# Kernel tuning notes

Hardware: AMD Instinct MI355X
Metric: run time of the kernel (lower is better)

The kernel has to match this reference:

```python
import jax, jax.numpy as jnp
import numpy as np

V = 49152      # HEALPix nside=64 pixel count
B = 2
FIN = 32
FOUT = 64
K = 8          # Chebyshev kernel_size
DEG = 8        # neighbors per pixel (plus self-loop -> 9 nnz/row)
G = 8          # GroupNorm num_groups
EPS = 1e-5
SLOPE = 0.1    # LeakyReLU negative slope


def setup_inputs() -> dict:
    key = jax.random.key(0)
    ks = jax.random.split(key, 4)
    rng = np.random.default_rng(0)
    # sparse Laplacian in COO: 8 random neighbors + self-loop per node
    row = np.repeat(np.arange(V, dtype=np.int32), DEG + 1)
    nbrs = rng.integers(0, V, size=(V, DEG))
    col = np.concatenate([nbrs, np.arange(V)[:, None]], axis=1).astype(np.int32).reshape(-1)
    vals = (rng.standard_normal(V * (DEG + 1)).astype(np.float32)) * 0.1
    x = jax.random.normal(ks[0], (B, V, FIN), dtype=jnp.float32)
    W1 = jax.random.normal(ks[1], (K, FIN, FOUT), dtype=jnp.float32) * 0.05
    W2 = jax.random.normal(ks[2], (K, FOUT, FOUT), dtype=jnp.float32) * 0.05
    Wr = jax.random.normal(ks[3], (K, FIN, FOUT), dtype=jnp.float32) * 0.05
    zeros = jnp.zeros((FOUT,), dtype=jnp.float32)
    ones = jnp.ones((FOUT,), dtype=jnp.float32)
    return {
        "x": x,
        "lap_vals": jnp.asarray(vals),
        "lap_row": jnp.asarray(row),
        "lap_col": jnp.asarray(col),
        "W1": W1, "b1": zeros, "g1": ones, "be1": zeros,
        "W2": W2, "b2": zeros, "g2": ones, "be2": zeros,
        "Wr": Wr, "br": zeros,
    }


def _spmm(vals, row, col, z):
    # L @ z for COO Laplacian; z: [V, D]
    return jax.ops.segment_sum(vals[:, None] * z[col], row, num_segments=V)


def _cheb_conv(x, vals, row, col, W, b):
    # x: [B, V, Fin], W: [K, Fin, Fout] -> [B, V, Fout]
    Bb, Vv, F = x.shape
    x0 = jnp.transpose(x, (1, 0, 2)).reshape(Vv, Bb * F)  # [V, B*F]
    xs = [x0, _spmm(vals, row, col, x0)]
    for _ in range(K - 2):
        xs.append(2.0 * _spmm(vals, row, col, xs[-1]) - xs[-2])
    Xk = jnp.stack(xs, 0).reshape(K, Vv, Bb, F)
    Xk = jnp.transpose(Xk, (2, 1, 0, 3))  # [B, V, K, F]
    return jnp.einsum('bvkf,kfo->bvo', Xk, W) + b


def _group_norm(x, gamma, beta):
    # equivalent to nn.GroupNorm applied on x.permute(0,2,1): normalize over (C/G, V)
    Bb, Vv, C = x.shape
    xg = x.reshape(Bb, Vv, G, C // G)
    mu = xg.mean(axis=(1, 3), keepdims=True)
    var = xg.var(axis=(1, 3), keepdims=True)
    xn = ((xg - mu) * jax.lax.rsqrt(var + EPS)).reshape(Bb, Vv, C)
    return xn * gamma + beta


def _block(x, vals, row, col, W, b, gamma, beta):
    h = _cheb_conv(x, vals, row, col, W, b)
    h = _group_norm(h, gamma, beta)
    return jax.nn.leaky_relu(h, SLOPE)  # out_channels > 1 -> LeakyReLU(0.1)


def reference(x, lap_vals, lap_row, lap_col, W1, b1, g1, be1, W2, b2, g2, be2, Wr, br):
    h = _block(x, lap_vals, lap_row, lap_col, W1, b1, g1, be1)
    h = _block(h, lap_vals, lap_row, lap_col, W2, b2, g2, be2)
    res = _cheb_conv(x, lap_vals, lap_row, lap_col, Wr, br)  # in != out -> res_conv
    return h + res
```

## Files before the change

kernel.cpp:

```cpp
#include <hip/hip_runtime.h>
#include <hip/hip_bf16.h>

#define V 49152
#define NNZ 9
#define EPSV 1e-5f
#define SLOPE 0.1f
#define RST 68

typedef __attribute__((ext_vector_type(8))) short bf16x8;
typedef __attribute__((ext_vector_type(4))) float f32x4;

__device__ __forceinline__ float lo2f(unsigned u) { return __uint_as_float(u << 16); }
__device__ __forceinline__ float hi2f(unsigned u) { return __uint_as_float(u & 0xffff0000u); }
__device__ __forceinline__ unsigned short f2us(float f) {
    __hip_bfloat16 h = __float2bfloat16(f);
    return *(unsigned short*)&h;
}
__device__ __forceinline__ unsigned pk2(float a, float b) {
    return ((unsigned)f2us(a)) | (((unsigned)f2us(b)) << 16);
}
__device__ __forceinline__ void fma8(float* t, float a, uint4 u) {
    t[0] += a * lo2f(u.x); t[1] += a * hi2f(u.x);
    t[2] += a * lo2f(u.y); t[3] += a * hi2f(u.y);
    t[4] += a * lo2f(u.z); t[5] += a * hi2f(u.z);
    t[6] += a * lo2f(u.w); t[7] += a * hi2f(u.w);
}
__device__ __forceinline__ void fold8(float* t, uint4 p) {
    t[0] = 2.f*t[0] - lo2f(p.x); t[1] = 2.f*t[1] - hi2f(p.x);
    t[2] = 2.f*t[2] - lo2f(p.y); t[3] = 2.f*t[3] - hi2f(p.y);
    t[4] = 2.f*t[4] - lo2f(p.z); t[5] = 2.f*t[5] - hi2f(p.z);
    t[6] = 2.f*t[6] - lo2f(p.w); t[7] = 2.f*t[7] - hi2f(p.w);
}
__device__ __forceinline__ uint4 pack8(const float* t) {
    uint4 r;
    r.x = pk2(t[0], t[1]); r.y = pk2(t[2], t[3]);
    r.z = pk2(t[4], t[5]); r.w = pk2(t[6], t[7]);
    return r;
}
__device__ __forceinline__ void gnleaky8(uint4 u, const float* scl, const float* sft, float* y) {
    float e[8] = { lo2f(u.x), hi2f(u.x), lo2f(u.y), hi2f(u.y),
                   lo2f(u.z), hi2f(u.z), lo2f(u.w), hi2f(u.w) };
    #pragma unroll
    for (int i = 0; i < 8; ++i) {
        float t = e[i] * scl[i] + sft[i];
        y[i] = t > 0.f ? t : SLOPE * t;
    }
}
__device__ __forceinline__ void gload_lds16(const void* g, void* l) {
    __builtin_amdgcn_global_load_lds((__attribute__((address_space(1))) void*)g,
                                     (__attribute__((address_space(3))) void*)l, 16, 0, 0);
}

__global__ __launch_bounds__(256) void prep_reorder_k(
    const float* __restrict__ x, unsigned* __restrict__ t0,
    const float* __restrict__ W1, const float* __restrict__ Wr, const float* __restrict__ W2,
    unsigned short* __restrict__ Wt1, unsigned short* __restrict__ Wtr, unsigned short* __restrict__ Wt2,
    float* __restrict__ part)
{
    int bid = blockIdx.x;
    if (bid < 6144) {
        int idx = bid * 256 + threadIdx.x;
        int v = idx >> 5, j2 = idx & 31;
        int b = j2 >> 4, f0 = (j2 & 15) * 2;
        const float* p = x + ((size_t)b * V + v) * 32 + f0;
        t0[idx] = pk2(p[0], p[1]);
    } else {
        int i = (bid - 6144) * 256 + threadIdx.x;
        if (i < 32768) {
            int kk = i >> 12, rem = i & 4095, o = rem >> 6, f = rem & 63;
            Wt2[i] = f2us(W2[kk * 4096 + f * 64 + o]);
        } else if (i < 49152) {
            int j = i - 32768;
            int kk = j >> 11, rem = j & 2047, o = rem >> 5, f = rem & 31;
            Wt1[j] = f2us(W1[kk * 2048 + f * 64 + o]);
        } else if (i < 65536) {
            int j = i - 49152;
            int kk = j >> 11, rem = j & 2047, o = rem >> 5, f = rem & 31;
            Wtr[j] = f2us(Wr[kk * 2048 + f * 64 + o]);
        } else if (i < 66560) {
            part[i - 65536] = 0.f;
        }
    }
}

template<int THR, bool FIRST>
__global__ __launch_bounds__(256) void spmm_step(
    const uint4* __restrict__ zc, const uint4* __restrict__ zp, uint4* __restrict__ zn,
    const float* __restrict__ vals, const int* __restrict__ col)
{
    constexpr int L4 = THR * 2;
    int tid = blockIdx.x * 256 + threadIdx.x;
    int v = tid / THR;
    int c = (tid - v * THR) * 2;
    int base = v * NNZ;
    float t[16];
    #pragma unroll
    for (int i = 0; i < 16; ++i) t[i] = 0.f;
    #pragma unroll
    for (int n = 0; n < NNZ; ++n) {
        float a = vals[base + n];
        int cc = col[base + n];
        const uint4* p = zc + (size_t)cc * L4 + c;
        fma8(t, a, p[0]);
        fma8(t + 8, a, p[1]);
    }
    if (!FIRST) {
        const uint4* pp = zp + (size_t)v * L4 + c;
        fold8(t, pp[0]);
        fold8(t + 8, pp[1]);
    }
    uint4* q = zn + (size_t)v * L4 + c;
    q[0] = pack8(t);
    q[1] = pack8(t + 8);
}

template<int MODE>
__global__ __launch_bounds__(256) void spmm2_gn(
    const unsigned short* __restrict__ ACC, const uint4* __restrict__ zc,
    uint4* __restrict__ zn, const float* __restrict__ part,
    const float* __restrict__ gamma, const float* __restrict__ beta,
    const float* __restrict__ vals, const int* __restrict__ col)
{
    int tid = blockIdx.x * 256 + threadIdx.x;
    int v = tid >> 3;
    int c2 = (tid & 7) * 2;
    int b = c2 >> 3;
    int ch0 = (c2 & 7) * 8;
    const float Nf = (float)V * 8.f;
    int g0 = c2 & 7;
    float m0 = part[(b*8+g0)*2] / Nf;
    float r0 = rsqrtf(part[(b*8+g0)*2+1]/Nf - m0*m0 + EPSV);
    float m1 = part[(b*8+g0+1)*2] / Nf;
    float r1 = rsqrtf(part[(b*8+g0+1)*2+1]/Nf - m1*m1 + EPSV);
    float scl[16], sft[16];
    #pragma unroll
    for (int i = 0; i < 8; ++i) {
        int o = ch0 + i;
        scl[i] = r0 * gamma[o];     sft[i] = beta[o] - m0 * scl[i];
        scl[8+i] = r1 * gamma[o+8]; sft[8+i] = beta[o+8] - m1 * scl[8+i];
    }

    float t[16];
    #pragma unroll
    for (int i = 0; i < 16; ++i) t[i] = 0.f;
    int base = v * NNZ;
    #pragma unroll
    for (int n = 0; n < NNZ; ++n) {
        float a = vals[base + n];
        int cc = col[base + n];
        if constexpr (MODE == 0) {
            const uint4* p = (const uint4*)(const void*)(ACC + ((size_t)b * V + cc) * 64 + ch0);
            float y[8];
            gnleaky8(p[0], scl, sft, y);
            #pragma unroll
            for (int i = 0; i < 8; ++i) t[i] += a * y[i];
            gnleaky8(p[1], scl + 8, sft + 8, y);
            #pragma unroll
            for (int i = 0; i < 8; ++i) t[8 + i] += a * y[i];
        } else {
            const uint4* p = zc + (size_t)cc * 16 + c2;
            fma8(t, a, p[0]);
            fma8(t + 8, a, p[1]);
        }
    }
    if constexpr (MODE == 1) {
        const uint4* pp = (const uint4*)(const void*)(ACC + ((size_t)b * V + v) * 64 + ch0);
        float y[8];
        gnleaky8(pp[0], scl, sft, y);
        #pragma unroll
        for (int i = 0; i < 8; ++i) t[i] = 2.f * t[i] - y[i];
        gnleaky8(pp[1], scl + 8, sft + 8, y);
        #pragma unroll
        for (int i = 0; i < 8; ++i) t[8 + i] = 2.f * t[8 + i] - y[i];
    }
    uint4* q = zn + (size_t)v * 16 + c2;
    q[0] = pack8(t);
    q[1] = pack8(t + 8);
}

__global__ __launch_bounds__(256) void gemm1f(
    const unsigned short* __restrict__ T,
    const unsigned short* __restrict__ WtA, const unsigned short* __restrict__ WtB,
    const float* __restrict__ biasA, const float* __restrict__ biasB,
    const float* __restrict__ vals, const int* __restrict__ col,
    unsigned short* __restrict__ ACC, float* __restrict__ resOut, float* __restrict__ part)
{
    __shared__ unsigned short shraw[34816];
    __shared__ float sGrp[32];
    unsigned short* tile = shraw;
    float* accbuf  = (float*)shraw;
    float* dualbuf = accbuf + 2 * 64 * RST;

    int wv = threadIdx.x >> 6, lane = threadIdx.x & 63;
    int quad = lane >> 4, l15 = lane & 15;
    int v0 = blockIdx.x * 64;
    int ot = wv;

    #pragma unroll
    for (int i = 0; i < 14; ++i) {
        int s = (i * 4 + wv) * 64 + lane;
        int kkl = s >> 9;
        int ws = s & 511;
        int row = ws >> 3;
        int cl = ws & 7;
        int cg = cl ^ (row & 7);
        const unsigned short* gp = T + ((size_t)kkl * V + v0 + row) * 64 + cg * 8;
        gload_lds16(gp, tile + (size_t)(i * 4 + wv) * 64 * 8);
    }

    {
        const unsigned short* T6 = T + (size_t)6 * V * 64;
        const unsigned short* T5 = T + (size_t)5 * V * 64;
        int row = threadIdx.x >> 2, c2 = (threadIdx.x & 3) * 2;
        int gv = v0 + row;
        float t[16];
        #pragma unroll
        for (int i = 0; i < 16; ++i) t[i] = 0.f;
        int base = gv * NNZ;
        #pragma unroll
        for (int n = 0; n < NNZ; ++n) {
            float a = vals[base + n];
            int cc = col[base + n];
            const uint4* p = (const uint4*)(const void*)(T6 + (size_t)cc * 64 + c2 * 8);
            fma8(t, a, p[0]);
            fma8(t + 8, a, p[1]);
        }
        const uint4* pp = (const uint4*)(const void*)(T5 + (size_t)gv * 64 + c2 * 8);
        fold8(t, pp[0]);
        fold8(t + 8, pp[1]);
        uint4* tl = (uint4*)tile;
        int r7 = row & 7;
        tl[(7 * 64 + row) * 8 + (c2 ^ r7)]       = pack8(t);
        tl[(7 * 64 + row) * 8 + ((c2 + 1) ^ r7)] = pack8(t + 8);
    }

    bf16x8 bw[8], bd[8];
    #pragma unroll
    for (int kk = 0; kk < 8; ++kk) {
        size_t brow = ((size_t)kk * 64 + ot * 16 + l15) * 32 + quad * 8;
        bw[kk] = *(const bf16x8*)(const void*)(WtA + brow);
        bd[kk] = *(const bf16x8*)(const void*)(WtB + brow);
    }
    f32x4 acc[4][2], accd[4][2];
    #pragma unroll
    for (int m = 0; m < 4; ++m)
        #pragma unroll
        for (int b = 0; b < 2; ++b) {
            acc[m][b]  = (f32x4){0.f, 0.f, 0.f, 0.f};
            accd[m][b] = (f32x4){0.f, 0.f, 0.f, 0.f};
        }
    __syncthreads();

    #pragma unroll
    for (int kk = 0; kk < 8; ++kk) {
        #pragma unroll
        for (int m = 0; m < 4; ++m) {
            int r = m * 16 + l15;
            int rx = r & 7;
            const unsigned short* rbase = tile + ((size_t)kk * 64 + r) * 64;
            #pragma unroll
            for (int b = 0; b < 2; ++b) {
                int s0 = (b * 4 + quad) ^ rx;
                bf16x8 a = *(const bf16x8*)(const void*)(rbase + s0 * 8);
                acc[m][b]  = __builtin_amdgcn_mfma_f32_16x16x32_bf16(a, bw[kk], acc[m][b], 0, 0, 0);
                accd[m][b] = __builtin_amdgcn_mfma_f32_16x16x32_bf16(a, bd[kk], accd[m][b], 0, 0, 0);
            }
        }
    }

    __syncthreads();
    int o = ot * 16 + l15;
    float biA = biasA[o], biB = biasB[o];
    #pragma unroll
    for (int m = 0; m < 4; ++m)
        #pragma unroll
        for (int b = 0; b < 2; ++b)
            #pragma unroll
            for (int rr = 0; rr < 4; ++rr) {
                int r = m * 16 + quad * 4 + rr;
                accbuf[(b * 64 + r) * RST + o] = acc[m][b][rr] + biA;
                dualbuf[(b * 64 + r) * RST + o] = accd[m][b][rr] + biB;
            }
    if (threadIdx.x < 32) sGrp[threadIdx.x] = 0.f;
    __syncthreads();
    #pragma unroll
    for (int j = 0; j < 4; ++j) {
        int cid = threadIdx.x + 256 * j;
        int g = cid & 7, r = (cid >> 3) & 63, b = cid >> 9;
        const float* src = accbuf + (b * 64 + r) * RST + g * 8;
        float e[8], s = 0.f, q = 0.f;
        #pragma unroll
        for (int i = 0; i < 8; ++i) { e[i] = src[i]; s += e[i]; q += e[i] * e[i]; }
        *(uint4*)(void*)(ACC + ((size_t)b * V + v0 + r) * 64 + g * 8) = pack8(e);
        atomicAdd(&sGrp[b * 8 + g], s);
        atomicAdd(&sGrp[16 + b * 8 + g], q);
    }
    #pragma unroll
    for (int j = 0; j < 8; ++j) {
        int cid = threadIdx.x + 256 * j;
        int oc = cid & 15, r = (cid >> 4) & 63, b = cid >> 10;
        float4 vv = *(const float4*)(const void*)(dualbuf + (b * 64 + r) * RST + oc * 4);
        *(float4*)(void*)(resOut + ((size_t)b * V + v0 + r) * 64 + oc * 4) = vv;
    }
    __syncthreads();
    if (threadIdx.x < 16) {
        atomicAdd(&part[threadIdx.x * 2],     sGrp[threadIdx.x]);
        atomicAdd(&part[threadIdx.x * 2 + 1], sGrp[16 + threadIdx.x]);
    }
}

__global__ __launch_bounds__(256) void gemm2f(
    const unsigned short* __restrict__ T,
    unsigned short* ACC,
    const float* __restrict__ part1, const float* __restrict__ g1, const float* __restrict__ be1,
    const unsigned short* __restrict__ Wt2, const float* __restrict__ biasA,
    float* __restrict__ part2,
    const float* __restrict__ vals, const int* __restrict__ col)
{
    __shared__ unsigned short shraw[32768];
    __shared__ float sGrp[32];
    unsigned short* tile = shraw;
    float* accbuf = (float*)shraw;

    int wv = threadIdx.x >> 6, lane = threadIdx.x & 63;
    int quad = lane >> 4, l15 = lane & 15;
    int v0 = blockIdx.x * 64;
    int ot = wv;
    const float Nf = (float)V * 8.f;

    #pragma unroll
    for (int i = 4; i < 16; ++i) {
        int s = (i * 4 + wv) * 64 + lane;
        int kkl = s >> 10;
        int ws = s & 1023;
        int row = ws >> 4;
        int cl = ws & 15;
        int cg = (cl & ~7) | ((cl & 7) ^ (row & 7));
        const unsigned short* gp = T + ((size_t)kkl * V + v0 + row) * 128 + cg * 8;
        gload_lds16(gp, tile + (size_t)(i * 4 + wv) * 64 * 8);
    }
    {
        int cl = threadIdx.x & 15;
        int b = cl >> 3, g = cl & 7, j8 = b * 8 + g;
        float mean = part1[j8 * 2] / Nf;
        float rstd = rsqrtf(part1[j8 * 2 + 1] / Nf - mean * mean + EPSV);
        int o0 = g * 8;
        float scl[8], sft[8];
        #pragma unroll
        for (int i = 0; i < 8; ++i) {
            scl[i] = rstd * g1[o0 + i];
            sft[i] = be1[o0 + i] - mean * scl[i];
        }
        uint4* tl = (uint4*)tile;
        #pragma unroll
        for (int j = 0; j < 4; ++j) {
            int r = (threadIdx.x >> 4) + 16 * j;
            uint4 aa = *(const uint4*)(const void*)(ACC + ((size_t)b * V + v0 + r) * 64 + o0);
            float y[8];
            gnleaky8(aa, scl, sft, y);
            tl[r * 16 + ((cl & ~7) | ((cl & 7) ^ (r & 7)))] = pack8(y);
        }
    }
    bf16x8 bw[8][2];
    #pragma unroll
    for (int kk = 0; kk < 8; ++kk)
        #pragma unroll
        for (int fh = 0; fh < 2; ++fh) {
            size_t brow = ((size_t)kk * 64 + ot * 16 + l15) * 64 + fh * 32 + quad * 8;
            bw[kk][fh] = *(const bf16x8*)(const void*)(Wt2 + brow);
        }
    f32x4 acc[4][2];
    #pragma unroll
    for (int m = 0; m < 4; ++m)
        #pragma unroll
        for (int b = 0; b < 2; ++b) acc[m][b] = (f32x4){0.f, 0.f, 0.f, 0.f};
    __syncthreads();

    #pragma unroll
    for (int kkl = 0; kkl < 4; ++kkl) {
        #pragma unroll
        for (int m = 0; m < 4; ++m) {
            int r = m * 16 + l15, rx = r & 7;
            const unsigned short* rbase = tile + ((size_t)kkl * 64 + r) * 128;
            #pragma unroll
            for (int b = 0; b < 2; ++b)
                #pragma unroll
                for (int fh = 0; fh < 2; ++fh) {
                    int c0 = b * 8 + fh * 4 + quad;
                    int s0 = (c0 & ~7) | ((c0 & 7) ^ rx);
                    bf16x8 a = *(const bf16x8*)(const void*)(rbase + s0 * 8);
                    acc[m][b] = __builtin_amdgcn_mfma_f32_16x16x32_bf16(a, bw[kkl][fh], acc[m][b], 0, 0, 0);
                }
        }
    }
    __syncthreads();

    #pragma unroll
    for (int i = 0; i < 12; ++i) {
        int s = (i * 4 + wv) * 64 + lane;
        int kkl = s >> 10;
        int ws = s & 1023;
        int row = ws >> 4;
        int cl = ws & 15;
        int cg = (cl & ~7) | ((cl & 7) ^ (row & 7));
        const unsigned short* gp = T + ((size_t)(4 + kkl) * V + v0 + row) * 128 + cg * 8;
        gload_lds16(gp, tile + (size_t)(i * 4 + wv) * 64 * 8);
    }
    {
        const unsigned short* T6 = T + (size_t)6 * V * 128;
        const unsigned short* T5 = T + (size_t)5 * V * 128;
        int row = threadIdx.x >> 2, cb = (threadIdx.x & 3) * 4;
        int gv = v0 + row;
        float t[32];
        #pragma unroll
        for (int i = 0; i < 32; ++i) t[i] = 0.f;
        int base = gv * NNZ;
        #pragma unroll
        for (int n = 0; n < NNZ; ++n) {
            float a = vals[base + n];
            int cc = col[base + n];
            const uint4* p = (const uint4*)(const void*)(T6 + (size_t)cc * 128 + cb * 8);
            fma8(t, a, p[0]);
            fma8(t + 8, a, p[1]);
            fma8(t + 16, a, p[2]);
            fma8(t + 24, a, p[3]);
        }
        const uint4* pp = (const uint4*)(const void*)(T5 + (size_t)gv * 128 + cb * 8);
        fold8(t, pp[0]);
        fold8(t + 8, pp[1]);
        fold8(t + 16, pp[2]);
        fold8(t + 24, pp[3]);
        uint4* tl = (uint4*)tile;
        int r7 = row & 7;
        #pragma unroll
        for (int q = 0; q < 4; ++q) {
            int c = cb + q;
            tl[(3 * 64 + row) * 16 + ((c & ~7) | ((c & 7) ^ r7))] = pack8(t + q * 8);
        }
    }
    __syncthreads();

    #pragma unroll
    for (int kkl = 0; kkl < 4; ++kkl) {
        int kk = 4 + kkl;
        #pragma unroll
        for (int m = 0; m < 4; ++m) {
            int r = m * 16 + l15, rx = r & 7;
            const unsigned short* rbase = tile + ((size_t)kkl * 64 + r) * 128;
            #pragma unroll
            for (int b = 0; b < 2; ++b)
                #pragma unroll
                for (int fh = 0; fh < 2; ++fh) {
                    int c0 = b * 8 + fh * 4 + quad;
                    int s0 = (c0 & ~7) | ((c0 & 7) ^ rx);
                    bf16x8 a = *(const bf16x8*)(const void*)(rbase + s0 * 8);
                    acc[m][b] = __builtin_amdgcn_mfma_f32_16x16x32_bf16(a, bw[kk][fh], acc[m][b], 0, 0, 0);
                }
        }
    }

    __syncthreads();
    int o = ot * 16 + l15;
    float biA = biasA[o];
    #pragma unroll
    for (int m = 0; m < 4; ++m)
        #pragma unroll
        for (int b = 0; b < 2; ++b)
            #pragma unroll
            for (int rr = 0; rr < 4; ++rr) {
                int r = m * 16 + quad * 4 + rr;
                accbuf[(b * 64 + r) * RST + o] = acc[m][b][rr] + biA;
            }
    if (threadIdx.x < 32) sGrp[threadIdx.x] = 0.f;
    __syncthreads();
    #pragma unroll
    for (int j = 0; j < 4; ++j) {
        int cid = threadIdx.x + 256 * j;
        int g = cid & 7, r = (cid >> 3) & 63, b = cid >> 9;
        const float* src = accbuf + (b * 64 + r) * RST + g * 8;
        float e[8], s = 0.f, q = 0.f;
        #pragma unroll
        for (int i = 0; i < 8; ++i) { e[i] = src[i]; s += e[i]; q += e[i] * e[i]; }
        *(uint4*)(void*)(ACC + ((size_t)b * V + v0 + r) * 64 + g * 8) = pack8(e);
        atomicAdd(&sGrp[b * 8 + g], s);
        atomicAdd(&sGrp[16 + b * 8 + g], q);
    }
    __syncthreads();
    if (threadIdx.x < 16) {
        atomicAdd(&part2[threadIdx.x * 2],     sGrp[threadIdx.x]);
        atomicAdd(&part2[threadIdx.x * 2 + 1], sGrp[16 + threadIdx.x]);
    }
}

__global__ __launch_bounds__(256) void final_out(const unsigned short* __restrict__ ACC,
                                                 float* outres,
                                                 const float* __restrict__ part,
                                                 const float* __restrict__ gamma, const float* __restrict__ beta) {
    int idx = blockIdx.x * 256 + threadIdx.x;
    int b = idx >= V * 8 ? 1 : 0;
    int r = idx - b * V * 8;
    int v = r >> 3, g = r & 7;
    int j = b * 8 + g;
    const float N = (float)V * 8.f;
    float mean = part[j * 2] / N;
    float rstd = rsqrtf(part[j * 2 + 1] / N - mean * mean + EPSV);
    int o0 = g * 8;
    size_t base = ((size_t)b * V + v) * 64 + o0;
    uint4 aa = *(const uint4*)(const void*)(ACC + base);
    float e[8] = { lo2f(aa.x), hi2f(aa.x), lo2f(aa.y), hi2f(aa.y),
                   lo2f(aa.z), hi2f(aa.z), lo2f(aa.w), hi2f(aa.w) };
    float4 r0 = *(const float4*)(const void*)(outres + base);
    float4 r1 = *(const float4*)(const void*)(outres + base + 4);
    float y[8];
    #pragma unroll
    for (int i = 0; i < 8; ++i) {
        float t = (e[i] - mean) * rstd * gamma[o0 + i] + beta[o0 + i];
        y[i] = t > 0.f ? t : SLOPE * t;
    }
    float4 w0 = { y[0] + r0.x, y[1] + r0.y, y[2] + r0.z, y[3] + r0.w };
    float4 w1 = { y[4] + r1.x, y[5] + r1.y, y[6] + r1.z, y[7] + r1.w };
    *(float4*)(void*)(outres + base) = w0;
    *(float4*)(void*)(outres + base + 4) = w1;
}

extern "C" void kernel_launch(void* const* d_in, const int* in_sizes, int n_in,
                              void* d_out, int out_size, void* d_ws, size_t ws_size,
                              hipStream_t stream) {
    const float* x    = (const float*)d_in[0];
    const float* vals = (const float*)d_in[1];
    const int*   col  = (const int*)d_in[3];
    const float* W1   = (const float*)d_in[4];
    const float* b1   = (const float*)d_in[5];
    const float* g1   = (const float*)d_in[6];
    const float* be1  = (const float*)d_in[7];
    const float* W2   = (const float*)d_in[8];
    const float* b2   = (const float*)d_in[9];
    const float* g2   = (const float*)d_in[10];
    const float* be2  = (const float*)d_in[11];
    const float* Wr   = (const float*)d_in[12];
    const float* br   = (const float*)d_in[13];
    float* out = (float*)d_out;

    unsigned short* TS  = (unsigned short*)d_ws;
    unsigned short* ACC = TS + (size_t)8 * V * 128;
    unsigned short* Wt1 = ACC + (size_t)2 * V * 64;
    unsigned short* Wtr = Wt1 + 8 * 64 * 32;
    unsigned short* Wt2 = Wtr + 8 * 64 * 32;
    float* PART1 = (float*)(Wt2 + 8 * 64 * 64);
    float* PART2 = PART1 + 32;

    prep_reorder_k<<<6404, 256, 0, stream>>>(x, (unsigned*)TS, W1, Wr, W2, Wt1, Wtr, Wt2, PART1);

    uint4* T1s[8];
    for (int k = 0; k < 8; ++k) T1s[k] = (uint4*)(TS + (size_t)k * V * 64);
    spmm_step<4, true><<<V * 4 / 256, 256, 0, stream>>>(T1s[0], nullptr, T1s[1], vals, col);
    for (int k = 2; k < 7; ++k)
        spmm_step<4, false><<<V * 4 / 256, 256, 0, stream>>>(T1s[k-1], T1s[k-2], T1s[k], vals, col);

    gemm1f<<<V / 64, 256, 0, stream>>>(TS, Wt1, Wtr, b1, br, vals, col, ACC, out, PART1);

    uint4* T2s[8];
    for (int k = 0; k < 8; ++k) T2s[k] = (uint4*)(TS + (size_t)k * V * 128);
    spmm2_gn<0><<<V * 8 / 256, 256, 0, stream>>>(ACC, nullptr, T2s[1], PART1, g1, be1, vals, col);
    spmm2_gn<1><<<V * 8 / 256, 256, 0, stream>>>(ACC, T2s[1], T2s[2], PART1, g1, be1, vals, col);
    for (int k = 3; k < 7; ++k)
        spmm_step<8, false><<<V * 8 / 256, 256, 0, stream>>>(T2s[k-1], T2s[k-2], T2s[k], vals, col);

    gemm2f<<<V / 64, 256, 0, stream>>>(TS, ACC, PART1, g1, be1, Wt2, b2, PART2, vals, col);

    final_out<<<2 * V * 8 / 256, 256, 0, stream>>>(ACC, out, PART2, g2, be2);
}
```

Before: 364.1 us.

## Split second-block Chebyshev buffers into channel planes and transpose Laplacian to SoA

```diff
diff --git a/kernel.cpp b/kernel.cpp
--- a/kernel.cpp
+++ b/kernel.cpp
@@ -55,7 +55,9 @@
     const float* __restrict__ x, unsigned* __restrict__ t0,
     const float* __restrict__ W1, const float* __restrict__ Wr, const float* __restrict__ W2,
     unsigned short* __restrict__ Wt1, unsigned short* __restrict__ Wtr, unsigned short* __restrict__ Wt2,
-    float* __restrict__ part)
+    float* __restrict__ part,
+    const float* __restrict__ vals, const int* __restrict__ col,
+    float* __restrict__ VT, int* __restrict__ CT)
 {
     int bid = blockIdx.x;
     if (bid < 6144) {
@@ -64,7 +66,7 @@
         int b = j2 >> 4, f0 = (j2 & 15) * 2;
         const float* p = x + ((size_t)b * V + v) * 32 + f0;
         t0[idx] = pk2(p[0], p[1]);
-    } else {
+    } else if (bid < 6404) {
         int i = (bid - 6144) * 256 + threadIdx.x;
         if (i < 32768) {
             int kk = i >> 12, rem = i & 4095, o = rem >> 6, f = rem & 63;
@@ -77,9 +79,14 @@
             int j = i - 49152;
             int kk = j >> 11, rem = j & 2047, o = rem >> 5, f = rem & 31;
             Wtr[j] = f2us(Wr[kk * 2048 + f * 64 + o]);
-        } else if (i < 66560) {
+        } else if (i < 65600) {
             part[i - 65536] = 0.f;
         }
+    } else {
+        int i = (bid - 6404) * 256 + threadIdx.x;
+        int n = i / V, v = i - n * V;
+        VT[i] = vals[v * NNZ + n];
+        CT[i] = col[v * NNZ + n];
     }
 }
 
@@ -114,68 +121,97 @@
     q[1] = pack8(t + 8);
 }
 
+__global__ __launch_bounds__(256) void spmm2p(
+    const unsigned short* __restrict__ zc, const unsigned short* __restrict__ zp,
+    unsigned short* __restrict__ zn,
+    const float* __restrict__ VT, const int* __restrict__ CT)
+{
+    int p = blockIdx.x & 7;
+    int v = (blockIdx.x >> 3) * 256 + threadIdx.x;
+    size_t pb = (size_t)p * V * 16;
+    float t[16];
+    #pragma unroll
+    for (int i = 0; i < 16; ++i) t[i] = 0.f;
+    #pragma unroll
+    for (int n = 0; n < NNZ; ++n) {
+        float a = VT[n * V + v];
+        int cc = CT[n * V + v];
+        const uint4* q = (const uint4*)(const void*)(zc + pb + (size_t)cc * 16);
+        fma8(t, a, q[0]);
+        fma8(t + 8, a, q[1]);
+    }
+    const uint4* pz = (const uint4*)(const void*)(zp + pb + (size_t)v * 16);
+    fold8(t, pz[0]);
+    fold8(t + 8, pz[1]);
+    uint4* o = (uint4*)(void*)(zn + pb + (size_t)v * 16);
+    o[0] = pack8(t);
+    o[1] = pack8(t + 8);
+}
+
 template<int MODE>
 __global__ __launch_bounds__(256) void spmm2_gn(
-    const unsigned short* __restrict__ ACC, const uint4* __restrict__ zc,
-    uint4* __restrict__ zn, const float* __restrict__ part,
+    const unsigned short* __restrict__ ACC, const unsigned short* __restrict__ zc,
+    unsigned short* __restrict__ zn, const float* __restrict__ part,
     const float* __restrict__ gamma, const float* __restrict__ beta,
-    const float* __restrict__ vals, const int* __restrict__ col)
+    const float* __restrict__ VT, const int* __restrict__ CT)
 {
-    int tid = blockIdx.x * 256 + threadIdx.x;
-    int v = tid >> 3;
-    int c2 = (tid & 7) * 2;
-    int b = c2 >> 3;
-    int ch0 = (c2 & 7) * 8;
+    int p = blockIdx.x & 7;
+    int v = (blockIdx.x >> 3) * 256 + threadIdx.x;
+    int b2 = p >> 2, g0 = (p & 3) * 2;
+    int j8 = b2 * 8 + g0;
     const float Nf = (float)V * 8.f;
-    int g0 = c2 & 7;
-    float m0 = part[(b*8+g0)*2] / Nf;
-    float r0 = rsqrtf(part[(b*8+g0)*2+1]/Nf - m0*m0 + EPSV);
-    float m1 = part[(b*8+g0+1)*2] / Nf;
-    float r1 = rsqrtf(part[(b*8+g0+1)*2+1]/Nf - m1*m1 + EPSV);
+    int o0 = g0 * 8;
+    float m0 = part[j8 * 2] / Nf;
+    float r0 = rsqrtf(part[j8 * 2 + 1] / Nf - m0 * m0 + EPSV);
+    float m1 = part[(j8 + 1) * 2] / Nf;
+    float r1 = rsqrtf(part[(j8 + 1) * 2 + 1] / Nf - m1 * m1 + EPSV);
     float scl[16], sft[16];
     #pragma unroll
     for (int i = 0; i < 8; ++i) {
-        int o = ch0 + i;
-        scl[i] = r0 * gamma[o];     sft[i] = beta[o] - m0 * scl[i];
-        scl[8+i] = r1 * gamma[o+8]; sft[8+i] = beta[o+8] - m1 * scl[8+i];
-    }
+        scl[i] = r0 * gamma[o0 + i];         sft[i] = beta[o0 + i] - m0 * scl[i];
+        scl[8 + i] = r1 * gamma[o0 + 8 + i]; sft[8 + i] = beta[o0 + 8 + i] - m1 * scl[8 + i];
+    }
+    size_t a0 = (size_t)j8 * V * 8;
+    size_t a1 = (size_t)(j8 + 1) * V * 8;
+    size_t pb = (size_t)p * V * 16;
 
     float t[16];
     #pragma unroll
     for (int i = 0; i < 16; ++i) t[i] = 0.f;
-    int base = v * NNZ;
     #pragma unroll
     for (int n = 0; n < NNZ; ++n) {
-        float a = vals[base + n];
-        int cc = col[base + n];
+        float a = VT[n * V + v];
+        int cc = CT[n * V + v];
         if constexpr (MODE == 0) {
-            const uint4* p = (const uint4*)(const void*)(ACC + ((size_t)b * V + cc) * 64 + ch0);
+            uint4 q0 = *(const uint4*)(const void*)(ACC + a0 + (size_t)cc * 8);
+            uint4 q1 = *(const uint4*)(const void*)(ACC + a1 + (size_t)cc * 8);
             float y[8];
-            gnleaky8(p[0], scl, sft, y);
+            gnleaky8(q0, scl, sft, y);
             #pragma unroll
             for (int i = 0; i < 8; ++i) t[i] += a * y[i];
-            gnleaky8(p[1], scl + 8, sft + 8, y);
+            gnleaky8(q1, scl + 8, sft + 8, y);
             #pragma unroll
             for (int i = 0; i < 8; ++i) t[8 + i] += a * y[i];
         } else {
-            const uint4* p = zc + (size_t)cc * 16 + c2;
-            fma8(t, a, p[0]);
-            fma8(t + 8, a, p[1]);
+            const uint4* q = (const uint4*)(const void*)(zc + pb + (size_t)cc * 16);
+            fma8(t, a, q[0]);
+            fma8(t + 8, a, q[1]);
         }
     }
     if constexpr (MODE == 1) {
-        const uint4* pp = (const uint4*)(const void*)(ACC + ((size_t)b * V + v) * 64 + ch0);
+        uint4 q0 = *(const uint4*)(const void*)(ACC + a0 + (size_t)v * 8);
+        uint4 q1 = *(const uint4*)(const void*)(ACC + a1 + (size_t)v * 8);
         float y[8];
-        gnleaky8(pp[0], scl, sft, y);
+        gnleaky8(q0, scl, sft, y);
         #pragma unroll
         for (int i = 0; i < 8; ++i) t[i] = 2.f * t[i] - y[i];
-        gnleaky8(pp[1], scl + 8, sft + 8, y);
+        gnleaky8(q1, scl + 8, sft + 8, y);
         #pragma unroll
         for (int i = 0; i < 8; ++i) t[8 + i] = 2.f * t[8 + i] - y[i];
     }
-    uint4* q = zn + (size_t)v * 16 + c2;
-    q[0] = pack8(t);
-    q[1] = pack8(t + 8);
+    uint4* o = (uint4*)(void*)(zn + pb + (size_t)v * 16);
+    o[0] = pack8(t);
+    o[1] = pack8(t + 8);
 }
 
 __global__ __launch_bounds__(256) void gemm1f(
@@ -291,7 +327,7 @@
         float e[8], s = 0.f, q = 0.f;
         #pragma unroll
         for (int i = 0; i < 8; ++i) { e[i] = src[i]; s += e[i]; q += e[i] * e[i]; }
-        *(uint4*)(void*)(ACC + ((size_t)b * V + v0 + r) * 64 + g * 8) = pack8(e);
+        *(uint4*)(void*)(ACC + ((size_t)(b * 8 + g) * V + v0 + r) * 8) = pack8(e);
         atomicAdd(&sGrp[b * 8 + g], s);
         atomicAdd(&sGrp[16 + b * 8 + g], q);
     }
@@ -315,7 +351,7 @@
     const float* __restrict__ part1, const float* __restrict__ g1, const float* __restrict__ be1,
     const unsigned short* __restrict__ Wt2, const float* __restrict__ biasA,
     float* __restrict__ part2,
-    const float* __restrict__ vals, const int* __restrict__ col)
+    const float* __restrict__ VT, const int* __restrict__ CT)
 {
     __shared__ unsigned short shraw[32768];
     __shared__ float sGrp[32];
@@ -336,7 +372,8 @@
         int row = ws >> 4;
         int cl = ws & 15;
         int cg = (cl & ~7) | ((cl & 7) ^ (row & 7));
-        const unsigned short* gp = T + ((size_t)kkl * V + v0 + row) * 128 + cg * 8;
+        const unsigned short* gp = T + (size_t)kkl * (V * 128) + (size_t)(cg >> 1) * (V * 16)
+                                     + (size_t)(v0 + row) * 16 + (cg & 1) * 8;
         gload_lds16(gp, tile + (size_t)(i * 4 + wv) * 64 * 8);
     }
     {
@@ -355,7 +392,7 @@
         #pragma unroll
         for (int j = 0; j < 4; ++j) {
             int r = (threadIdx.x >> 4) + 16 * j;
-            uint4 aa = *(const uint4*)(const void*)(ACC + ((size_t)b * V + v0 + r) * 64 + o0);
+            uint4 aa = *(const uint4*)(const void*)(ACC + ((size_t)j8 * V + v0 + r) * 8);
             float y[8];
             gnleaky8(aa, scl, sft, y);
             tl[r * 16 + ((cl & ~7) | ((cl & 7) ^ (r & 7)))] = pack8(y);
@@ -403,7 +440,8 @@
         int row = ws >> 4;
         int cl = ws & 15;
         int cg = (cl & ~7) | ((cl & 7) ^ (row & 7));
-        const unsigned short* gp = T + ((size_t)(4 + kkl) * V + v0 + row) * 128 + cg * 8;
+        const unsigned short* gp = T + (size_t)(4 + kkl) * (V * 128) + (size_t)(cg >> 1) * (V * 16)
+                                     + (size_t)(v0 + row) * 16 + (cg & 1) * 8;
         gload_lds16(gp, tile + (size_t)(i * 4 + wv) * 64 * 8);
     }
     {
@@ -411,25 +449,23 @@
         const unsigned short* T5 = T + (size_t)5 * V * 128;
         int row = threadIdx.x >> 2, cb = (threadIdx.x & 3) * 4;
         int gv = v0 + row;
+        size_t pA = (size_t)(cb >> 1) * (V * 16), pB = pA + V * 16;
         float t[32];
         #pragma unroll
         for (int i = 0; i < 32; ++i) t[i] = 0.f;
-        int base = gv * NNZ;
         #pragma unroll
         for (int n = 0; n < NNZ; ++n) {
-            float a = vals[base + n];
-            int cc = col[base + n];
-            const uint4* p = (const uint4*)(const void*)(T6 + (size_t)cc * 128 + cb * 8);
-            fma8(t, a, p[0]);
-            fma8(t + 8, a, p[1]);
-            fma8(t + 16, a, p[2]);
-            fma8(t + 24, a, p[3]);
-        }
-        const uint4* pp = (const uint4*)(const void*)(T5 + (size_t)gv * 128 + cb * 8);
-        fold8(t, pp[0]);
-        fold8(t + 8, pp[1]);
-        fold8(t + 16, pp[2]);
-        fold8(t + 24, pp[3]);
+            float a = VT[n * V + gv];
+            int cc = CT[n * V + gv];
+            const uint4* qa = (const uint4*)(const void*)(T6 + pA + (size_t)cc * 16);
+            const uint4* qb = (const uint4*)(const void*)(T6 + pB + (size_t)cc * 16);
+            fma8(t, a, qa[0]);       fma8(t + 8, a, qa[1]);
+            fma8(t + 16, a, qb[0]);  fma8(t + 24, a, qb[1]);
+        }
+        const uint4* za = (const uint4*)(const void*)(T5 + pA + (size_t)gv * 16);
+        const uint4* zb = (const uint4*)(const void*)(T5 + pB + (size_t)gv * 16);
+        fold8(t, za[0]);       fold8(t + 8, za[1]);
+        fold8(t + 16, zb[0]);  fold8(t + 24, zb[1]);
         uint4* tl = (uint4*)tile;
         int r7 = row & 7;
         #pragma unroll
@@ -481,7 +517,7 @@
         float e[8], s = 0.f, q = 0.f;
         #pragma unroll
         for (int i = 0; i < 8; ++i) { e[i] = src[i]; s += e[i]; q += e[i] * e[i]; }
-        *(uint4*)(void*)(ACC + ((size_t)b * V + v0 + r) * 64 + g * 8) = pack8(e);
+        *(uint4*)(void*)(ACC + ((size_t)(b * 8 + g) * V + v0 + r) * 8) = pack8(e);
         atomicAdd(&sGrp[b * 8 + g], s);
         atomicAdd(&sGrp[16 + b * 8 + g], q);
     }
@@ -505,10 +541,10 @@
     float mean = part[j * 2] / N;
     float rstd = rsqrtf(part[j * 2 + 1] / N - mean * mean + EPSV);
     int o0 = g * 8;
-    size_t base = ((size_t)b * V + v) * 64 + o0;
-    uint4 aa = *(const uint4*)(const void*)(ACC + base);
+    uint4 aa = *(const uint4*)(const void*)(ACC + ((size_t)j * V + v) * 8);
     float e[8] = { lo2f(aa.x), hi2f(aa.x), lo2f(aa.y), hi2f(aa.y),
                    lo2f(aa.z), hi2f(aa.z), lo2f(aa.w), hi2f(aa.w) };
+    size_t base = ((size_t)b * V + v) * 64 + o0;
     float4 r0 = *(const float4*)(const void*)(outres + base);
     float4 r1 = *(const float4*)(const void*)(outres + base + 4);
     float y[8];
@@ -548,8 +584,11 @@
     unsigned short* Wt2 = Wtr + 8 * 64 * 32;
     float* PART1 = (float*)(Wt2 + 8 * 64 * 64);
     float* PART2 = PART1 + 32;
-
-    prep_reorder_k<<<6404, 256, 0, stream>>>(x, (unsigned*)TS, W1, Wr, W2, Wt1, Wtr, Wt2, PART1);
+    float* VT = PART2 + 32;
+    int* CT = (int*)(VT + (size_t)NNZ * V);
+
+    prep_reorder_k<<<8132, 256, 0, stream>>>(x, (unsigned*)TS, W1, Wr, W2, Wt1, Wtr, Wt2,
+                                             PART1, vals, col, VT, CT);
 
     uint4* T1s[8];
     for (int k = 0; k < 8; ++k) T1s[k] = (uint4*)(TS + (size_t)k * V * 64);
@@ -559,14 +598,14 @@
 
     gemm1f<<<V / 64, 256, 0, stream>>>(TS, Wt1, Wtr, b1, br, vals, col, ACC, out, PART1);
 
-    uint4* T2s[8];
-    for (int k = 0; k < 8; ++k) T2s[k] = (uint4*)(TS + (size_t)k * V * 128);
-    spmm2_gn<0><<<V * 8 / 256, 256, 0, stream>>>(ACC, nullptr, T2s[1], PART1, g1, be1, vals, col);
-    spmm2_gn<1><<<V * 8 / 256, 256, 0, stream>>>(ACC, T2s[1], T2s[2], PART1, g1, be1, vals, col);
+    unsigned short* T2s[8];
+    for (int k = 0; k < 8; ++k) T2s[k] = TS + (size_t)k * V * 128;
+    spmm2_gn<0><<<1536, 256, 0, stream>>>(ACC, nullptr, T2s[1], PART1, g1, be1, VT, CT);
+    spmm2_gn<1><<<1536, 256, 0, stream>>>(ACC, T2s[1], T2s[2], PART1, g1, be1, VT, CT);
     for (int k = 3; k < 7; ++k)
-        spmm_step<8, false><<<V * 8 / 256, 256, 0, stream>>>(T2s[k-1], T2s[k-2], T2s[k], vals, col);
-
-    gemm2f<<<V / 64, 256, 0, stream>>>(TS, ACC, PART1, g1, be1, Wt2, b2, PART2, vals, col);
+        spmm2p<<<1536, 256, 0, stream>>>(T2s[k-1], T2s[k-2], T2s[k], VT, CT);
+
+    gemm2f<<<V / 64, 256, 0, stream>>>(TS, ACC, PART1, g1, be1, Wt2, b2, PART2, VT, CT);
 
     final_out<<<2 * V * 8 / 256, 256, 0, stream>>>(ACC, out, PART2, g2, be2);
 }
```

After: 444.8 us. 1.22x slower.
